# Performance work log

Hardware: AMD Instinct MI355X
Metric: run time of the kernel (lower is better)

## Reference

```python
import jax, jax.numpy as jnp
import numpy as np

NUM_ITERATIONS = 3


def squash(s, axis=-1):
    # s * sqrt(||s||^2) / (1 + ||s||^2), matching the torch source exactly
    sq = jnp.sum(s * s, axis=axis, keepdims=True)
    return s * jnp.sqrt(sq) / (1.0 + sq)


def setup_inputs() -> dict:
    key = jax.random.key(0)
    k_u, k_w = jax.random.split(key)
    B, J, R, O, I = 128, 166, 864, 8, 4
    u = jax.random.normal(k_u, (B, R, I), dtype=jnp.float32)
    W = jax.random.normal(k_w, (1, J, R, O, I), dtype=jnp.float32)
    return {"u": u, "W": W}


def reference(u, W):
    # u: [B, R, I]; W: [1, J, R, O, I]
    Wq = W[0]  # [J, R, O, I]
    # u_hat[b,j,r,o] = sum_i W[j,r,o,i] * u[b,r,i]
    u_hat = jnp.einsum('jroi,bri->bjro', Wq, u)  # [B, J, R, O]
    # routing logits start shared across batch (torch init: [1,J,R,1,1])
    b_ij = jnp.zeros((1, Wq.shape[0], Wq.shape[1]), dtype=u_hat.dtype)  # [1, J, R]
    v_j = None
    for it in range(NUM_ITERATIONS):
        c_ij = jax.nn.softmax(b_ij, axis=2)           # softmax over routes R
        s_j = jnp.einsum('bjr,bjro->bjo', jnp.broadcast_to(c_ij, u_hat.shape[:3]), u_hat)  # [B, J, O]
        v_j = squash(s_j, axis=-1)                    # [B, J, O]
        if it < NUM_ITERATIONS - 1:
            # agreement a[b,j,r] = <u_hat[b,j,r,:], v[b,j,:]>
            a_ij = jnp.einsum('bjro,bjo->bjr', u_hat, v_j)
            b_ij = b_ij + a_ij                        # broadcasts to [B, J, R]
    return v_j  # equivalent to torch v_j.squeeze() for B > 1
```

## Files before the change

### kernel.cpp

```cpp
#include <hip/hip_runtime.h>
#include <math.h>


#define BB 128
#define JJ 166
#define RR 864
#define OO 8
#define KMAX 14
#define WP_U2 (JJ * 7168)
#define UP_U2 (BB * 896)

typedef __fp16 h2v __attribute__((ext_vector_type(2)));

static __device__ __forceinline__ uint32_t pack2(float a, float b) {
    return __builtin_bit_cast(uint32_t, __builtin_amdgcn_cvt_pkrtz(a, b));
}
static __device__ __forceinline__ h2v bc_h2(uint32_t u) {
    return __builtin_bit_cast(h2v, u);
}
static __device__ __forceinline__ float lo_f(uint32_t u) {
    return (float)__builtin_bit_cast(h2v, u).x;
}
static __device__ __forceinline__ float hi_f(uint32_t u) {
    return (float)__builtin_bit_cast(h2v, u).y;
}

static __device__ __forceinline__ float dpp_wave_sum(float x) {
#define DPP_STEP(CTRL)                                                         \
    x += __builtin_bit_cast(                                                   \
        float, __builtin_amdgcn_update_dpp(0, __builtin_bit_cast(int, x),      \
                                           (CTRL), 0xF, 0xF, true));
    DPP_STEP(0x111)
    DPP_STEP(0x112)
    DPP_STEP(0x114)
    DPP_STEP(0x118)
    DPP_STEP(0x142)
    DPP_STEP(0x143)
#undef DPP_STEP
    return __builtin_bit_cast(
        float, __builtin_amdgcn_readlane(__builtin_bit_cast(int, x), 63));
}

__global__ __launch_bounds__(256) void prepack_kernel(
    const float* __restrict__ u, const float* __restrict__ W,
    uint2* __restrict__ ws) {
    const int t = threadIdx.x;
    const int bid = blockIdx.x;
    if (bid < JJ * 7) {
        const int j = bid / 7;
        const int c = bid - j * 7;
        const float4* __restrict__ W4 = (const float4*)W;
        uint2* __restrict__ dst = ws + (size_t)bid * 1024;
#pragma unroll
        for (int i = 0; i < 4; ++i) {
            const int e = i * 256 + t;
            const int o = e >> 7;
            const int rl = e & 127;
            const int r = c * 128 + rl;
            float4 w = make_float4(0.f, 0.f, 0.f, 0.f);
            if (r < RR) w = W4[((size_t)j * RR + r) * 8 + o];
            dst[e] = make_uint2(pack2(w.x, w.y), pack2(w.z, w.w));
        }
    } else {
        const int e = (bid - JJ * 7) * 256 + t;
        const int b = e / 896;
        const int r = e - b * 896;
        const float4* __restrict__ u4 = (const float4*)u;
        float4 uu = make_float4(0.f, 0.f, 0.f, 0.f);
        if (r < RR) uu = u4[(size_t)b * RR + r];
        ws[WP_U2 + e] = make_uint2(pack2(uu.x, uu.y), pack2(uu.z, uu.w));
    }
}

__global__ __launch_bounds__(256) void digitcaps_kernel(
    const uint2* __restrict__ Wp, const uint2* __restrict__ uP,
    float* __restrict__ out) {
    const int tid = threadIdx.x;
    const int lane = tid & 63;
    const int wave = tid >> 6;

    int bid = blockIdx.x;
    bid = (bid & 7) * 664 + (bid >> 3);
    const int j = bid >> 5;
    const int b = ((bid & 31) << 2) + wave;

    __shared__ uint2 wlds[2][1024];

    const uint2* __restrict__ uPb = uP + (size_t)b * 896;

    uint32_t uh[KMAX][4];

#define STAGE(CC, BUF)                                                         \
    {                                                                          \
        const char* gsrc = (const char*)(Wp + ((size_t)j * 7 + (CC)) * 1024);  \
        _Pragma("unroll")                                                      \
        for (int i = 0; i < 2; ++i) {                                          \
            __builtin_amdgcn_global_load_lds(                                  \
                (const __attribute__((address_space(1))) uint32_t*)            \
                    (gsrc + i * 4096 + tid * 16),                              \
                (__attribute__((address_space(3))) uint32_t*)                  \
                    ((char*)(&wlds[BUF][0]) + i * 4096 + (wave << 10)),        \
                16, 0, 0);                                                     \
        }                                                                      \
    }

#define COMPUTE(CC, BUF)                                                       \
    {                                                                          \
        _Pragma("unroll")                                                      \
        for (int kl = 0; kl < 2; ++kl) {                                       \
            const int rl = (kl << 6) + lane;                                   \
            const uint2 up = uPb[(CC) * 128 + rl];                             \
            float d[OO];                                                       \
            _Pragma("unroll")                                                  \
            for (int o = 0; o < OO; ++o) {                                     \
                const uint2 ww = wlds[BUF][o * 128 + rl];                      \
                float t0 = __builtin_amdgcn_fdot2(bc_h2(ww.x), bc_h2(up.x),    \
                                                  0.0f, false);                \
                d[o] = __builtin_amdgcn_fdot2(bc_h2(ww.y), bc_h2(up.y), t0,    \
                                              false);                          \
            }                                                                  \
            _Pragma("unroll")                                                  \
            for (int o2 = 0; o2 < 4; ++o2)                                     \
                uh[(CC) * 2 + kl][o2] = pack2(d[2 * o2], d[2 * o2 + 1]);       \
        }                                                                      \
    }

    STAGE(0, 0)
    __syncthreads();
    STAGE(1, 1) COMPUTE(0, 0)
    __syncthreads();
    STAGE(2, 0) COMPUTE(1, 1)
    __syncthreads();
    STAGE(3, 1) COMPUTE(2, 0)
    __syncthreads();
    STAGE(4, 0) COMPUTE(3, 1)
    __syncthreads();
    STAGE(5, 1) COMPUTE(4, 0)
    __syncthreads();
    STAGE(6, 0) COMPUTE(5, 1)
    __syncthreads();
    COMPUTE(6, 0)
#undef STAGE
#undef COMPUTE

    float V[OO];
    float v[OO];

    {
        h2v accp[4];
#pragma unroll
        for (int o2 = 0; o2 < 4; ++o2) accp[o2] = bc_h2(uh[0][o2]);
#pragma unroll
        for (int k = 1; k < KMAX; ++k)
#pragma unroll
            for (int o2 = 0; o2 < 4; ++o2) accp[o2] += bc_h2(uh[k][o2]);

        float s[OO];
#pragma unroll
        for (int o2 = 0; o2 < 4; ++o2) {
            s[2 * o2]     = dpp_wave_sum((float)accp[o2].x) * (1.0f / (float)RR);
            s[2 * o2 + 1] = dpp_wave_sum((float)accp[o2].y) * (1.0f / (float)RR);
        }
        float n2 = 0.0f;
#pragma unroll
        for (int o = 0; o < OO; ++o) n2 += s[o] * s[o];
        const float scale = sqrtf(n2) / (1.0f + n2);
#pragma unroll
        for (int o = 0; o < OO; ++o) { v[o] = s[o] * scale; V[o] = v[o]; }
    }

#pragma unroll
    for (int it = 1; it < 3; ++it) {
        uint32_t Vp[4];
#pragma unroll
        for (int o2 = 0; o2 < 4; ++o2)
            Vp[o2] = pack2(V[2 * o2], V[2 * o2 + 1]);

        float zp = 0.0f;
        float sp[OO];
#pragma unroll
        for (int o = 0; o < OO; ++o) sp[o] = 0.0f;

#pragma unroll
        for (int k = 0; k < KMAX; ++k) {
            float br = 0.0f;
#pragma unroll
            for (int o2 = 0; o2 < 4; ++o2)
                br = __builtin_amdgcn_fdot2(bc_h2(uh[k][o2]), bc_h2(Vp[o2]),
                                            br, false);
            const float e = (k < KMAX - 1 || lane < 32) ? __expf(br) : 0.0f;
            zp += e;
#pragma unroll
            for (int o2 = 0; o2 < 4; ++o2) {
                sp[2 * o2]     = fmaf(e, lo_f(uh[k][o2]), sp[2 * o2]);
                sp[2 * o2 + 1] = fmaf(e, hi_f(uh[k][o2]), sp[2 * o2 + 1]);
            }
        }
        const float invZ = 1.0f / dpp_wave_sum(zp);

        float s[OO];
#pragma unroll
        for (int o = 0; o < OO; ++o) s[o] = dpp_wave_sum(sp[o]) * invZ;

        float n2 = 0.0f;
#pragma unroll
        for (int o = 0; o < OO; ++o) n2 += s[o] * s[o];
        const float scale = sqrtf(n2) / (1.0f + n2);
#pragma unroll
        for (int o = 0; o < OO; ++o) v[o] = s[o] * scale;

        if (it < 2) {
#pragma unroll
            for (int o = 0; o < OO; ++o) V[o] += v[o];
        }
    }

    float outv = 0.0f;
#pragma unroll
    for (int o = 0; o < OO; ++o)
        if (lane == o) outv = v[o];
    if (lane < OO) out[(b * JJ + j) * OO + lane] = outv;
}

extern "C" void kernel_launch(void* const* d_in, const int* in_sizes, int n_in,
                              void* d_out, int out_size, void* d_ws, size_t ws_size,
                              hipStream_t stream) {
    const float* u = (const float*)d_in[0];
    const float* W = (const float*)d_in[1];
    float* out = (float*)d_out;
    uint2* ws = (uint2*)d_ws;

    prepack_kernel<<<JJ * 7 + (BB * 896) / 256, 256, 0, stream>>>(u, W, ws);

    digitcaps_kernel<<<JJ * 32, 256, 0, stream>>>(ws, ws + WP_U2, out);
}
```

Baseline: 131.5 us.

## Interleave W output pairs in LDS and deepen staging to four buffers

The prepack now interleaves adjacent output channels per route, so each lane reads two channels with one 16-byte LDS load instead of two 8-byte loads. The LDS staging grows from two to four buffers, and loads are issued two chunks ahead, which cuts the number of block barriers from seven to four. The aim is fewer LDS instructions and more latency hiding for the global-to-LDS loads. The cost is doubled LDS use per block (32 KB), which may lower occupancy, and wider LDS reads may hit bank conflicts.

```diff
diff --git a/kernel.cpp b/kernel.cpp
--- a/kernel.cpp
+++ b/kernel.cpp
@@ -54,8 +54,10 @@
 #pragma unroll
         for (int i = 0; i < 4; ++i) {
             const int e = i * 256 + t;
-            const int o = e >> 7;
-            const int rl = e & 127;
+            const int op = e >> 8;
+            const int rl = (e & 255) >> 1;
+            const int p = e & 1;
+            const int o = 2 * op + p;
             const int r = c * 128 + rl;
             float4 w = make_float4(0.f, 0.f, 0.f, 0.f);
             if (r < RR) w = W4[((size_t)j * RR + r) * 8 + o];
@@ -84,7 +86,7 @@
     const int j = bid >> 5;
     const int b = ((bid & 31) << 2) + wave;
 
-    __shared__ uint2 wlds[2][1024];
+    __shared__ uint2 wlds[4][1024];
 
     const uint2* __restrict__ uPb = uP + (size_t)b * 896;
 
@@ -110,36 +112,34 @@
         for (int kl = 0; kl < 2; ++kl) {                                       \
             const int rl = (kl << 6) + lane;                                   \
             const uint2 up = uPb[(CC) * 128 + rl];                             \
-            float d[OO];                                                       \
             _Pragma("unroll")                                                  \
-            for (int o = 0; o < OO; ++o) {                                     \
-                const uint2 ww = wlds[BUF][o * 128 + rl];                      \
+            for (int op = 0; op < 4; ++op) {                                   \
+                const uint4 ww =                                               \
+                    *(const uint4*)(&wlds[BUF][op * 256 + (rl << 1)]);         \
                 float t0 = __builtin_amdgcn_fdot2(bc_h2(ww.x), bc_h2(up.x),    \
                                                   0.0f, false);                \
-                d[o] = __builtin_amdgcn_fdot2(bc_h2(ww.y), bc_h2(up.y), t0,    \
-                                              false);                          \
+                const float d0 = __builtin_amdgcn_fdot2(bc_h2(ww.y),           \
+                                                        bc_h2(up.y), t0,      \
+                                                        false);               \
+                float t1 = __builtin_amdgcn_fdot2(bc_h2(ww.z), bc_h2(up.x),    \
+                                                  0.0f, false);                \
+                const float d1 = __builtin_amdgcn_fdot2(bc_h2(ww.w),           \
+                                                        bc_h2(up.y), t1,      \
+                                                        false);               \
+                uh[(CC) * 2 + kl][op] = pack2(d0, d1);                         \
             }                                                                  \
-            _Pragma("unroll")                                                  \
-            for (int o2 = 0; o2 < 4; ++o2)                                     \
-                uh[(CC) * 2 + kl][o2] = pack2(d[2 * o2], d[2 * o2 + 1]);       \
         }                                                                      \
     }
 
-    STAGE(0, 0)
-    __syncthreads();
-    STAGE(1, 1) COMPUTE(0, 0)
-    __syncthreads();
-    STAGE(2, 0) COMPUTE(1, 1)
-    __syncthreads();
-    STAGE(3, 1) COMPUTE(2, 0)
-    __syncthreads();
-    STAGE(4, 0) COMPUTE(3, 1)
-    __syncthreads();
-    STAGE(5, 1) COMPUTE(4, 0)
-    __syncthreads();
-    STAGE(6, 0) COMPUTE(5, 1)
-    __syncthreads();
-    COMPUTE(6, 0)
+    STAGE(0, 0) STAGE(1, 1) STAGE(2, 2)
+    __syncthreads();
+    STAGE(3, 3) COMPUTE(0, 0) COMPUTE(1, 1)
+    __syncthreads();
+    STAGE(4, 0) STAGE(5, 1) COMPUTE(2, 2) COMPUTE(3, 3)
+    __syncthreads();
+    STAGE(6, 2) COMPUTE(4, 0) COMPUTE(5, 1)
+    __syncthreads();
+    COMPUTE(6, 2)
 #undef STAGE
 #undef COMPUTE
 
```

After: 124.9 us. -5.0%, faster.
